# Performance work log

Hardware: AMD Instinct MI355X
Metric: run time of the kernel (lower is better)

## Reference

```python
import jax, jax.numpy as jnp
import numpy as np

B, T, TREF, C, H = 2, 2048, 512, 768, 12
D = C // H


def setup_inputs() -> dict:
    key = jax.random.key(0)
    ks = jax.random.split(key, 20)
    s = 0.02  # init scale for weights
    inp = {
        "x": jax.random.normal(ks[0], (B, T, C), dtype=jnp.float32),
        "mask": jax.random.randint(ks[1], (B, 1, T, T), 0, 2, dtype=jnp.int32),
        "rel_pos": jax.random.normal(ks[2], (H, T, T), dtype=jnp.float32) * 0.1,
        "ref_feat": jax.random.normal(ks[3], (B, TREF, C), dtype=jnp.float32),
    }
    names = ["Wq", "Wk", "Wv", "Wrk", "Wrv", "Wo"]
    for i, n in enumerate(names):
        inp[n] = jax.random.normal(ks[4 + i], (C, C), dtype=jnp.float32) * s
        inp["b" + n[1:]] = jnp.zeros((C,), dtype=jnp.float32)
    return inp


def _heads(t, W, b):
    # nn.Linear: y = t @ W.T + b, then (B, L, H, D) -> (B, H, L, D)
    Bt, L, _ = t.shape
    return (t @ W.T + b).reshape(Bt, L, H, D).transpose(0, 2, 1, 3)


def reference(x, mask, rel_pos, ref_feat, Wq, bq, Wk, bk, Wv, bv,
              Wrk, brk, Wrv, brv, Wo, bo):
    Bx, Tx, Cx = x.shape
    Tref = ref_feat.shape[1]
    q = _heads(x, Wq, bq)                  # (B,H,T,D)
    k = _heads(x, Wk, bk)
    v = _heads(x, Wv, bv)
    rk = _heads(ref_feat, Wrk, brk)        # (B,H,Tref,D)
    rv = _heads(ref_feat, Wrv, brv)
    k = jnp.concatenate([k, rk], axis=2)   # (B,H,T+Tref,D)
    v = jnp.concatenate([v, rv], axis=2)
    # additive bias: -inf where mask==1 (self keys), rel_pos on self keys,
    # ref keys get 0 bias (mask padded with 0)
    bias_self = jnp.where(mask == 1, -jnp.inf, 0.0).astype(x.dtype) + rel_pos[None]  # (B,H,T,T)
    bias = jnp.pad(bias_self, ((0, 0), (0, 0), (0, 0), (0, Tref)))  # (B,H,T,T+Tref)
    scale = 1.0 / jnp.sqrt(jnp.asarray(D, dtype=x.dtype))
    scores = jnp.einsum('bhqd,bhkd->bhqk', q, k) * scale + bias
    attn = jax.nn.softmax(scores, axis=-1)
    y = jnp.einsum('bhqk,bhkd->bhqd', attn, v)
    y = y.transpose(0, 2, 1, 3).reshape(Bx, Tx, Cx)
    return y @ Wo.T + bo
```

## Files before the change

kernel.cpp:

```cpp
#include <hip/hip_runtime.h>


typedef __bf16 bf16x8 __attribute__((ext_vector_type(8)));
typedef float floatx4 __attribute__((ext_vector_type(4)));

__device__ __forceinline__ ushort f2bf(float f) {
  uint u = __builtin_bit_cast(uint, f);
  return (ushort)((u + 0x7FFFu + ((u >> 16) & 1u)) >> 16);
}
__device__ __forceinline__ float bf2f(ushort u) {
  return __builtin_bit_cast(float, (uint)u << 16);
}

__device__ __forceinline__ void gld16(ushort* lds, const ushort* g) {
  __builtin_amdgcn_global_load_lds(
      (const __attribute__((address_space(1))) unsigned int*)g,
      (__attribute__((address_space(3))) unsigned int*)lds, 16, 0, 0);
}

__global__ __launch_bounds__(256) void cast_all(
    const float* __restrict__ x, const float* __restrict__ rf,
    const float* __restrict__ w0, const float* __restrict__ w1,
    const float* __restrict__ w2, const float* __restrict__ w3,
    const float* __restrict__ w4, const float* __restrict__ w5,
    ushort* __restrict__ dst) {
  size_t i4 = ((size_t)blockIdx.x * 256 + threadIdx.x) * 4;
  const float* src;
  size_t off;
  if (i4 < 3145728) { src = x; off = i4; }
  else if (i4 < 3932160) { src = rf; off = i4 - 3145728; }
  else {
    size_t r = i4 - 3932160;
    if (r < 589824) { src = w0; off = r; }
    else if (r < 2 * 589824) { src = w1; off = r - 589824; }
    else if (r < 3 * 589824) { src = w2; off = r - 2 * 589824; }
    else if (r < 4 * 589824) { src = w3; off = r - 3 * 589824; }
    else if (r < 5 * 589824) { src = w4; off = r - 4 * 589824; }
    else { src = w5; off = r - 5 * 589824; }
  }
  float4 v = *(const float4*)(src + off);
  ushort4 o;
  o.x = f2bf(v.x); o.y = f2bf(v.y); o.z = f2bf(v.z); o.w = f2bf(v.w);
  *(ushort4*)(dst + i4) = o;
}

__global__ __launch_bounds__(256) void pack_mask(
    const int* __restrict__ mask, unsigned long long* __restrict__ bits) {
  const int gid = blockIdx.x * 256 + threadIdx.x;
  const int4* src = (const int4*)(mask + (size_t)gid * 64);
  unsigned long long v = 0;
#pragma unroll
  for (int j = 0; j < 16; ++j) {
    int4 m = src[j];
    unsigned long long nib = (m.x ? 1ull : 0ull) | (m.y ? 2ull : 0ull) |
                             (m.z ? 4ull : 0ull) | (m.w ? 8ull : 0ull);
    v |= nib << (j * 4);
  }
  bits[gid] = v;
}

__device__ __forceinline__ void gemm_core(
    const ushort* __restrict__ Ab, const ushort* __restrict__ Bb,
    ushort* As, ushort* Bs, int tid, int quad, int l16, int mw, int nw,
    floatx4 acc[4][4]) {
  const int w = tid >> 6;
  const int r0 = tid >> 2, kp = (tid & 3) * 8;
  const size_t ga0 = (size_t)r0 * 768 + kp;
  const size_t ga1 = ga0 + (size_t)64 * 768;
#define GEMM_ISSUE(kb, p)                                   \
  do {                                                      \
    const int k0_ = (kb) * 32;                              \
    gld16(&As[(p) * 4096 + w * 512], Ab + ga0 + k0_);       \
    gld16(&As[(p) * 4096 + w * 512 + 2048], Ab + ga1 + k0_);\
    gld16(&Bs[(p) * 4096 + w * 512], Bb + ga0 + k0_);       \
    gld16(&Bs[(p) * 4096 + w * 512 + 2048], Bb + ga1 + k0_);\
  } while (0)
  GEMM_ISSUE(0, 0);
#pragma unroll 1
  for (int kb = 0; kb < 24; ++kb) {
    __syncthreads();
    if (kb < 23) GEMM_ISSUE(kb + 1, (kb + 1) & 1);
    const int p = kb & 1;
    bf16x8 af[4], bfr[4];
#pragma unroll
    for (int mt = 0; mt < 4; ++mt)
      af[mt] = *(const bf16x8*)&As[p * 4096 + (mw + mt * 16 + l16) * 32 + quad * 8];
#pragma unroll
    for (int nt = 0; nt < 4; ++nt)
      bfr[nt] = *(const bf16x8*)&Bs[p * 4096 + (nw + nt * 16 + l16) * 32 + quad * 8];
#pragma unroll
    for (int mt = 0; mt < 4; ++mt)
#pragma unroll
      for (int nt = 0; nt < 4; ++nt)
        acc[mt][nt] = __builtin_amdgcn_mfma_f32_16x16x32_bf16(af[mt], bfr[nt], acc[mt][nt], 0, 0, 0);
  }
#undef GEMM_ISSUE
}

template <int REF>
__global__ __launch_bounds__(256) void gemm_fused(
    const ushort* __restrict__ A, const ushort* __restrict__ W,
    const float* __restrict__ bA, const float* __restrict__ bB,
    const float* __restrict__ bC,
    ushort* __restrict__ oA, ushort* __restrict__ oB, ushort* __restrict__ oC) {
  const int bm = blockIdx.x, bn = blockIdx.y;
  const int tid = threadIdx.x;
  const int w = tid >> 6, lane = tid & 63, quad = lane >> 4, l16 = lane & 15;
  const int mw = (w >> 1) * 64, nw = (w & 1) * 64;

  __shared__ __align__(16) ushort As[2 * 4096];
  __shared__ __align__(16) ushort Bs[2 * 4096];

  floatx4 acc[4][4];
#pragma unroll
  for (int mt = 0; mt < 4; ++mt)
#pragma unroll
    for (int nt = 0; nt < 4; ++nt) acc[mt][nt] = (floatx4){0.f, 0.f, 0.f, 0.f};

  gemm_core(A + (size_t)bm * 128 * 768, W + (size_t)bn * 128 * 768,
            As, Bs, tid, quad, l16, mw, nw, acc);

  const int sec = bn / 6;
  const float* bp = sec == 0 ? bA : sec == 1 ? bB : bC;
  ushort* op = sec == 0 ? oA : sec == 1 ? oB : oC;
  const bool qlay = (REF == 0 && sec == 0);
#pragma unroll
  for (int nt = 0; nt < 4; ++nt) {
    const int nloc = (bn - sec * 6) * 128 + nw + nt * 16 + l16;
    const float bv = bp[nloc];
    const int hh = nloc >> 6, dd = nloc & 63;
#pragma unroll
    for (int mt = 0; mt < 4; ++mt)
#pragma unroll
      for (int i = 0; i < 4; ++i) {
        const int m = bm * 128 + mw + mt * 16 + quad * 4 + i;
        int bb, tt;
        if (REF == 0) { bb = m >> 11; tt = m & 2047; }
        else { bb = m >> 9; tt = (m & 511) + 2048; }
        const size_t idx = qlay ? (((size_t)(bb * 12 + hh) * 2048 + tt) * 64 + dd)
                                : (((size_t)(bb * 12 + hh) * 2560 + tt) * 64 + dd);
        op[idx] = f2bf(acc[mt][nt][i] + bv);
      }
  }
}

__global__ __launch_bounds__(256) void gemm_out(
    const ushort* __restrict__ A, const ushort* __restrict__ W,
    const float* __restrict__ bias, float* __restrict__ out) {
  const int bm = blockIdx.x, bn = blockIdx.y;
  const int tid = threadIdx.x;
  const int w = tid >> 6, lane = tid & 63, quad = lane >> 4, l16 = lane & 15;
  const int mw = (w >> 1) * 64, nw = (w & 1) * 64;

  __shared__ __align__(16) ushort As[2 * 4096];
  __shared__ __align__(16) ushort Bs[2 * 4096];

  floatx4 acc[4][4];
#pragma unroll
  for (int mt = 0; mt < 4; ++mt)
#pragma unroll
    for (int nt = 0; nt < 4; ++nt) acc[mt][nt] = (floatx4){0.f, 0.f, 0.f, 0.f};

  gemm_core(A + (size_t)bm * 128 * 768, W + (size_t)bn * 128 * 768,
            As, Bs, tid, quad, l16, mw, nw, acc);

#pragma unroll
  for (int nt = 0; nt < 4; ++nt) {
    const int n = bn * 128 + nw + nt * 16 + l16;
    const float bv = bias[n];
#pragma unroll
    for (int mt = 0; mt < 4; ++mt)
#pragma unroll
      for (int i = 0; i < 4; ++i) {
        const int m = bm * 128 + mw + mt * 16 + quad * 4 + i;
        out[(size_t)m * 768 + n] = acc[mt][nt][i] + bv;
      }
  }
}

__global__ __launch_bounds__(256, 3) void attn(
    const ushort* __restrict__ qb, const ushort* __restrict__ kb,
    const ushort* __restrict__ vb, const unsigned long long* __restrict__ bits,
    const float* __restrict__ relp, ushort* __restrict__ yb) {
  const int b = blockIdx.x, qt = blockIdx.y, h = blockIdx.z;
  const int tid = threadIdx.x;
  const int w = tid >> 6, lane = tid & 63, quad = lane >> 4, l16 = lane & 15;

  __shared__ __align__(16) ushort Kl[2][64 * 64];
  __shared__ __align__(16) ushort Vl[2][64 * 64];
  __shared__ __align__(16) ushort Rel[64 * 72];
  __shared__ __align__(16) ushort Ps[4][16 * 72];

  const ushort* qsrc = qb + ((size_t)(b * 12 + h) * 2048 + qt * 64) * 64;
  const ushort* ksrc = kb + (size_t)(b * 12 + h) * 2560 * 64;
  const ushort* vsrc = vb + (size_t)(b * 12 + h) * 2560 * 64;
  const int qrow = qt * 64 + w * 16 + l16;
  const unsigned long long* brow = bits + ((size_t)b * 2048 + qrow) * 32;
  const float* rbase = relp + ((size_t)h * 2048 + qt * 64) * 2048;

  const int krow = lane >> 3;
  const int kchunk = (lane & 7) ^ krow;

#pragma unroll
  for (int c = 0; c < 2; ++c) {
    const int f = tid + c * 256;
    *(uint4*)&Vl[1][(f >> 3) * 64 + (f & 7) * 8] = *(const uint4*)(qsrc + f * 8);
  }
#pragma unroll
  for (int c = 0; c < 2; ++c) {
    const int rb = w * 16 + c * 8;
    gld16(&Kl[0][rb * 64], ksrc + (rb + krow) * 64 + kchunk * 8);
  }
  uint4 vd[2];
  float4 rd[4];
  unsigned long long bnext;
  vd[0] = *(const uint4*)(vsrc + tid * 8);
  vd[1] = *(const uint4*)(vsrc + (tid + 256) * 8);
#pragma unroll
  for (int p = 0; p < 4; ++p) {
    const int idx = lane + p * 64, rr = idx >> 4, c4 = idx & 15;
    rd[p] = *(const float4*)(rbase + (size_t)(w * 16 + rr) * 2048 + c4 * 4);
  }
  bnext = brow[0];

  __syncthreads();
  bf16x8 bQ[2];
  bQ[0] = *(const bf16x8*)&Vl[1][(w * 16 + l16) * 64 + quad * 8];
  bQ[1] = *(const bf16x8*)&Vl[1][(w * 16 + l16) * 64 + 32 + quad * 8];

  floatx4 acc[4];
#pragma unroll
  for (int mt = 0; mt < 4; ++mt) acc[mt] = (floatx4){0.f, 0.f, 0.f, 0.f};
  float m_run = -__builtin_inff(), l_run = 0.f;

#pragma unroll 1
  for (int it = 0; it < 40; ++it) {
    const int p = it & 1;
    const bool self = it < 32;
#pragma unroll
    for (int c = 0; c < 2; ++c) {
      const int f = tid + c * 256;
      const int key = f >> 3, d0 = (f & 7) * 8;
      const int cb = (((key >> 3) ^ (f & 7)) & 7) * 8 + (key & 7);
      uint vv[4] = {vd[c].x, vd[c].y, vd[c].z, vd[c].w};
#pragma unroll
      for (int u = 0; u < 4; ++u) {
        Vl[p][(d0 + 2 * u) * 64 + cb] = (ushort)(vv[u] & 0xffffu);
        Vl[p][(d0 + 2 * u + 1) * 64 + cb] = (ushort)(vv[u] >> 16);
      }
    }
    if (self) {
#pragma unroll
      for (int pp = 0; pp < 4; ++pp) {
        const int idx = lane + pp * 64, rr = idx >> 4, c4 = idx & 15;
        ushort4 o;
        o.x = f2bf(rd[pp].x); o.y = f2bf(rd[pp].y);
        o.z = f2bf(rd[pp].z); o.w = f2bf(rd[pp].w);
        *(ushort4*)&Rel[(w * 16 + rr) * 72 + c4 * 4] = o;
      }
    }
    const unsigned long long bcur = bnext;
    __syncthreads();

    const int itn = it + 1;
    if (itn < 40) {
#pragma unroll
      for (int c = 0; c < 2; ++c) {
        const int rb = w * 16 + c * 8;
        gld16(&Kl[itn & 1][rb * 64], ksrc + (size_t)itn * 4096 + (rb + krow) * 64 + kchunk * 8);
      }
      const ushort* vt0 = vsrc + (size_t)itn * 4096;
      vd[0] = *(const uint4*)(vt0 + tid * 8);
      vd[1] = *(const uint4*)(vt0 + (tid + 256) * 8);
      if (itn < 32) {
#pragma unroll
        for (int pp = 0; pp < 4; ++pp) {
          const int idx = lane + pp * 64, rr = idx >> 4, c4 = idx & 15;
          rd[pp] = *(const float4*)(rbase + (size_t)(w * 16 + rr) * 2048 + itn * 64 + c4 * 4);
        }
        bnext = brow[itn];
      }
    }

    floatx4 st[4];
#pragma unroll
    for (int mt = 0; mt < 4; ++mt) st[mt] = (floatx4){0.f, 0.f, 0.f, 0.f};
#pragma unroll
    for (int kk = 0; kk < 2; ++kk)
#pragma unroll
      for (int mt = 0; mt < 4; ++mt) {
        const bf16x8 aK = *(const bf16x8*)
            &Kl[p][(mt * 16 + l16) * 64 + (((kk * 4 + quad) ^ (l16 & 7)) * 8)];
        st[mt] = __builtin_amdgcn_mfma_f32_16x16x32_bf16(aK, bQ[kk], st[mt], 0, 0, 0);
      }
#pragma unroll
    for (int mt = 0; mt < 4; ++mt) {
      if (self) {
        const ushort4 rv4 = *(const ushort4*)&Rel[(w * 16 + l16) * 72 + mt * 16 + quad * 4];
        const ushort rv[4] = {rv4.x, rv4.y, rv4.z, rv4.w};
#pragma unroll
        for (int i = 0; i < 4; ++i) {
          const float sv = st[mt][i] * 0.125f + bf2f(rv[i]);
          const int bit = mt * 16 + quad * 4 + i;
          st[mt][i] = ((bcur >> bit) & 1ull) ? -__builtin_inff() : sv;
        }
      } else {
#pragma unroll
        for (int i = 0; i < 4; ++i) st[mt][i] *= 0.125f;
      }
    }
    float tm = st[0][0];
#pragma unroll
    for (int mt = 0; mt < 4; ++mt)
#pragma unroll
      for (int i = 0; i < 4; ++i) tm = fmaxf(tm, st[mt][i]);
    tm = fmaxf(tm, __shfl_xor(tm, 16));
    tm = fmaxf(tm, __shfl_xor(tm, 32));
    const float mnew = fmaxf(m_run, tm);
    const float mref = (mnew == -__builtin_inff()) ? 0.f : mnew;
    const float alpha = (m_run == -__builtin_inff()) ? 0.f : __expf(m_run - mnew);
    float rs = 0.f;
#pragma unroll
    for (int mt = 0; mt < 4; ++mt)
#pragma unroll
      for (int i = 0; i < 4; ++i) {
        const float pv = __expf(st[mt][i] - mref);
        st[mt][i] = pv;
        rs += pv;
      }
    rs += __shfl_xor(rs, 16);
    rs += __shfl_xor(rs, 32);
    l_run = l_run * alpha + rs;
    m_run = mnew;
#pragma unroll
    for (int mt = 0; mt < 4; ++mt)
#pragma unroll
      for (int i = 0; i < 4; ++i) acc[mt][i] *= alpha;

    {
      ushort* pw = &Ps[w][l16 * 72 + quad * 4];
#pragma unroll
      for (int mt = 0; mt < 4; ++mt) {
        const uint pk0 = (uint)f2bf(st[mt][0]) | ((uint)f2bf(st[mt][1]) << 16);
        const uint pk1 = (uint)f2bf(st[mt][2]) | ((uint)f2bf(st[mt][3]) << 16);
        *(uint*)&pw[mt * 16] = pk0;
        *(uint*)&pw[mt * 16 + 2] = pk1;
      }
    }
#pragma unroll
    for (int kk = 0; kk < 2; ++kk) {
      const bf16x8 bP = *(const bf16x8*)&Ps[w][l16 * 72 + kk * 32 + quad * 8];
#pragma unroll
      for (int mt = 0; mt < 4; ++mt) {
        const int dd = mt * 16 + l16;
        const int cs = (((kk * 4 + quad) ^ (dd >> 3)) & 7) * 8;
        const bf16x8 aV = *(const bf16x8*)&Vl[p][dd * 64 + cs];
        acc[mt] = __builtin_amdgcn_mfma_f32_16x16x32_bf16(aV, bP, acc[mt], 0, 0, 0);
      }
    }
  }

  const float inv = 1.f / l_run;
  ushort* yrow = yb + ((size_t)b * 2048 + qt * 64 + w * 16 + l16) * 768 + h * 64;
#pragma unroll
  for (int mt = 0; mt < 4; ++mt)
#pragma unroll
    for (int i = 0; i < 4; ++i)
      yrow[mt * 16 + quad * 4 + i] = f2bf(acc[mt][i] * inv);
}

extern "C" void kernel_launch(void* const* d_in, const int* in_sizes, int n_in,
                              void* d_out, int out_size, void* d_ws, size_t ws_size,
                              hipStream_t stream) {
  const float* x = (const float*)d_in[0];
  const int* mask = (const int*)d_in[1];
  const float* relp = (const float*)d_in[2];
  const float* ref = (const float*)d_in[3];
  const float* Wq = (const float*)d_in[4];
  const float* bq = (const float*)d_in[5];
  const float* Wk = (const float*)d_in[6];
  const float* bk = (const float*)d_in[7];
  const float* Wv = (const float*)d_in[8];
  const float* bv = (const float*)d_in[9];
  const float* Wrk = (const float*)d_in[10];
  const float* brk = (const float*)d_in[11];
  const float* Wrv = (const float*)d_in[12];
  const float* brv = (const float*)d_in[13];
  const float* Wo = (const float*)d_in[14];
  const float* bo = (const float*)d_in[15];

  ushort* xb = (ushort*)d_ws;
  ushort* refb = xb + 3145728;
  ushort* wb = refb + 786432;
  ushort* qbuf = wb + 6 * 589824;
  ushort* kbuf = qbuf + 3145728;
  ushort* vbuf = kbuf + 3932160;
  ushort* ybuf = vbuf + 3932160;
  unsigned long long* bitsbuf = (unsigned long long*)(ybuf + 3145728);

  cast_all<<<7296, 256, 0, stream>>>(x, ref, Wq, Wk, Wv, Wrk, Wrv, Wo, xb);
  pack_mask<<<512, 256, 0, stream>>>(mask, bitsbuf);

  gemm_fused<0><<<dim3(32, 18), 256, 0, stream>>>(
      xb, wb, bq, bk, bv, qbuf, kbuf, vbuf);
  gemm_fused<1><<<dim3(8, 12), 256, 0, stream>>>(
      refb, wb + (size_t)3 * 589824, brk, brv, nullptr, kbuf, vbuf, nullptr);

  attn<<<dim3(2, 32, 12), 256, 0, stream>>>(qbuf, kbuf, vbuf, bitsbuf, relp, ybuf);

  gemm_out<<<dim3(32, 6), 256, 0, stream>>>(
      ybuf, wb + (size_t)5 * 589824, bo, (float*)d_out);
}
```

Before: 474.2 us.

## Store V transposed in projection, fold softmax scale into Q, use exp2 with lazy rescale

The QKV projection epilogue now writes V in a transposed (head, d, token) layout, so the attention kernel can load V tiles straight into LDS with async global_load_lds instead of scattering them through registers. Q is pre-multiplied by scale*log2(e), so the scores go directly to exp2, and rel_pos is read per lane from global memory instead of being staged as bf16 in LDS. Online-softmax rescaling is skipped when the running max grows by at most 8, which saves the exp and the accumulator multiplies but lets unnormalized values grow larger in float. The P tile layout in LDS is also reorganized, and the Q tile is loaded directly from global memory.

Measured after the change: 488.6 us. 3.0% more time.

```diff
diff --git a/kernel.cpp b/kernel.cpp
--- a/kernel.cpp
+++ b/kernel.cpp
@@ -3,13 +3,25 @@
 
 typedef __bf16 bf16x8 __attribute__((ext_vector_type(8)));
 typedef float floatx4 __attribute__((ext_vector_type(4)));
+typedef uint uintx2 __attribute__((ext_vector_type(2)));
 
 __device__ __forceinline__ ushort f2bf(float f) {
   uint u = __builtin_bit_cast(uint, f);
   return (ushort)((u + 0x7FFFu + ((u >> 16) & 1u)) >> 16);
 }
-__device__ __forceinline__ float bf2f(ushort u) {
-  return __builtin_bit_cast(float, (uint)u << 16);
+
+__device__ __forceinline__ uint pack2bf(float lo, float hi) {
+  ushort a = __builtin_bit_cast(ushort, (__bf16)lo);
+  ushort b = __builtin_bit_cast(ushort, (__bf16)hi);
+  return (uint)a | ((uint)b << 16);
+}
+
+__device__ __forceinline__ float fexp2(float x) {
+#if __has_builtin(__builtin_amdgcn_exp2f)
+  return __builtin_amdgcn_exp2f(x);
+#else
+  return exp2f(x);
+#endif
 }
 
 __device__ __forceinline__ void gld16(ushort* lds, const ushort* g) {
@@ -124,23 +136,41 @@
   const float* bp = sec == 0 ? bA : sec == 1 ? bB : bC;
   ushort* op = sec == 0 ? oA : sec == 1 ? oB : oC;
   const bool qlay = (REF == 0 && sec == 0);
+  const bool vlay = (REF == 0) ? (sec == 2) : (sec == 1);
+  const float scl = qlay ? 0.18033688011112042f : 1.0f;
 #pragma unroll
   for (int nt = 0; nt < 4; ++nt) {
     const int nloc = (bn - sec * 6) * 128 + nw + nt * 16 + l16;
     const float bv = bp[nloc];
     const int hh = nloc >> 6, dd = nloc & 63;
-#pragma unroll
-    for (int mt = 0; mt < 4; ++mt)
-#pragma unroll
-      for (int i = 0; i < 4; ++i) {
-        const int m = bm * 128 + mw + mt * 16 + quad * 4 + i;
-        int bb, tt;
-        if (REF == 0) { bb = m >> 11; tt = m & 2047; }
-        else { bb = m >> 9; tt = (m & 511) + 2048; }
-        const size_t idx = qlay ? (((size_t)(bb * 12 + hh) * 2048 + tt) * 64 + dd)
-                                : (((size_t)(bb * 12 + hh) * 2560 + tt) * 64 + dd);
-        op[idx] = f2bf(acc[mt][nt][i] + bv);
-      }
+    if (vlay) {
+#pragma unroll
+      for (int mt = 0; mt < 4; ++mt) {
+        const int m0 = bm * 128 + mw + mt * 16 + quad * 4;
+        int bb, t0;
+        if (REF == 0) { bb = m0 >> 11; t0 = m0 & 2047; }
+        else { bb = m0 >> 9; t0 = (m0 & 511) + 2048; }
+        ushort4 o;
+        o.x = f2bf(acc[mt][nt][0] + bv);
+        o.y = f2bf(acc[mt][nt][1] + bv);
+        o.z = f2bf(acc[mt][nt][2] + bv);
+        o.w = f2bf(acc[mt][nt][3] + bv);
+        *(ushort4*)&op[((size_t)(bb * 12 + hh) * 64 + dd) * 2560 + t0] = o;
+      }
+    } else {
+#pragma unroll
+      for (int mt = 0; mt < 4; ++mt)
+#pragma unroll
+        for (int i = 0; i < 4; ++i) {
+          const int m = bm * 128 + mw + mt * 16 + quad * 4 + i;
+          int bb, tt;
+          if (REF == 0) { bb = m >> 11; tt = m & 2047; }
+          else { bb = m >> 9; tt = (m & 511) + 2048; }
+          const size_t idx = qlay ? (((size_t)(bb * 12 + hh) * 2048 + tt) * 64 + dd)
+                                  : (((size_t)(bb * 12 + hh) * 2560 + tt) * 64 + dd);
+          op[idx] = f2bf((acc[mt][nt][i] + bv) * scl);
+        }
+    }
   }
 }
 
@@ -186,47 +216,36 @@
   const int tid = threadIdx.x;
   const int w = tid >> 6, lane = tid & 63, quad = lane >> 4, l16 = lane & 15;
 
-  __shared__ __align__(16) ushort Kl[2][64 * 64];
-  __shared__ __align__(16) ushort Vl[2][64 * 64];
-  __shared__ __align__(16) ushort Rel[64 * 72];
-  __shared__ __align__(16) ushort Ps[4][16 * 72];
+  __shared__ __align__(16) ushort Kl[2][4096];
+  __shared__ __align__(16) ushort Vtl[2][4096];
+  __shared__ __align__(16) ushort Ps[4][8][16][8];
 
   const ushort* qsrc = qb + ((size_t)(b * 12 + h) * 2048 + qt * 64) * 64;
   const ushort* ksrc = kb + (size_t)(b * 12 + h) * 2560 * 64;
-  const ushort* vsrc = vb + (size_t)(b * 12 + h) * 2560 * 64;
+  const ushort* vtsrc = vb + (size_t)(b * 12 + h) * 64 * 2560;
   const int qrow = qt * 64 + w * 16 + l16;
   const unsigned long long* brow = bits + ((size_t)b * 2048 + qrow) * 32;
-  const float* rbase = relp + ((size_t)h * 2048 + qt * 64) * 2048;
+  const float* rrow = relp + ((size_t)h * 2048 + qrow) * 2048;
 
   const int krow = lane >> 3;
   const int kchunk = (lane & 7) ^ krow;
 
-#pragma unroll
-  for (int c = 0; c < 2; ++c) {
-    const int f = tid + c * 256;
-    *(uint4*)&Vl[1][(f >> 3) * 64 + (f & 7) * 8] = *(const uint4*)(qsrc + f * 8);
-  }
 #pragma unroll
   for (int c = 0; c < 2; ++c) {
     const int rb = w * 16 + c * 8;
     gld16(&Kl[0][rb * 64], ksrc + (rb + krow) * 64 + kchunk * 8);
-  }
-  uint4 vd[2];
+    gld16(&Vtl[0][rb * 64], vtsrc + (size_t)(rb + krow) * 2560 + kchunk * 8);
+  }
+
+  bf16x8 bQ[2];
+  bQ[0] = *(const bf16x8*)(qsrc + (w * 16 + l16) * 64 + quad * 8);
+  bQ[1] = *(const bf16x8*)(qsrc + (w * 16 + l16) * 64 + 32 + quad * 8);
+
   float4 rd[4];
-  unsigned long long bnext;
-  vd[0] = *(const uint4*)(vsrc + tid * 8);
-  vd[1] = *(const uint4*)(vsrc + (tid + 256) * 8);
-#pragma unroll
-  for (int p = 0; p < 4; ++p) {
-    const int idx = lane + p * 64, rr = idx >> 4, c4 = idx & 15;
-    rd[p] = *(const float4*)(rbase + (size_t)(w * 16 + rr) * 2048 + c4 * 4);
-  }
-  bnext = brow[0];
-
-  __syncthreads();
-  bf16x8 bQ[2];
-  bQ[0] = *(const bf16x8*)&Vl[1][(w * 16 + l16) * 64 + quad * 8];
-  bQ[1] = *(const bf16x8*)&Vl[1][(w * 16 + l16) * 64 + 32 + quad * 8];
+#pragma unroll
+  for (int mt = 0; mt < 4; ++mt)
+    rd[mt] = *(const float4*)(rrow + mt * 16 + quad * 4);
+  unsigned long long bnext = brow[0];
 
   floatx4 acc[4];
 #pragma unroll
@@ -237,48 +256,19 @@
   for (int it = 0; it < 40; ++it) {
     const int p = it & 1;
     const bool self = it < 32;
-#pragma unroll
-    for (int c = 0; c < 2; ++c) {
-      const int f = tid + c * 256;
-      const int key = f >> 3, d0 = (f & 7) * 8;
-      const int cb = (((key >> 3) ^ (f & 7)) & 7) * 8 + (key & 7);
-      uint vv[4] = {vd[c].x, vd[c].y, vd[c].z, vd[c].w};
-#pragma unroll
-      for (int u = 0; u < 4; ++u) {
-        Vl[p][(d0 + 2 * u) * 64 + cb] = (ushort)(vv[u] & 0xffffu);
-        Vl[p][(d0 + 2 * u + 1) * 64 + cb] = (ushort)(vv[u] >> 16);
-      }
-    }
-    if (self) {
-#pragma unroll
-      for (int pp = 0; pp < 4; ++pp) {
-        const int idx = lane + pp * 64, rr = idx >> 4, c4 = idx & 15;
-        ushort4 o;
-        o.x = f2bf(rd[pp].x); o.y = f2bf(rd[pp].y);
-        o.z = f2bf(rd[pp].z); o.w = f2bf(rd[pp].w);
-        *(ushort4*)&Rel[(w * 16 + rr) * 72 + c4 * 4] = o;
-      }
-    }
     const unsigned long long bcur = bnext;
     __syncthreads();
 
     const int itn = it + 1;
     if (itn < 40) {
+      const int pn = itn & 1;
 #pragma unroll
       for (int c = 0; c < 2; ++c) {
         const int rb = w * 16 + c * 8;
-        gld16(&Kl[itn & 1][rb * 64], ksrc + (size_t)itn * 4096 + (rb + krow) * 64 + kchunk * 8);
-      }
-      const ushort* vt0 = vsrc + (size_t)itn * 4096;
-      vd[0] = *(const uint4*)(vt0 + tid * 8);
-      vd[1] = *(const uint4*)(vt0 + (tid + 256) * 8);
-      if (itn < 32) {
-#pragma unroll
-        for (int pp = 0; pp < 4; ++pp) {
-          const int idx = lane + pp * 64, rr = idx >> 4, c4 = idx & 15;
-          rd[pp] = *(const float4*)(rbase + (size_t)(w * 16 + rr) * 2048 + itn * 64 + c4 * 4);
-        }
-        bnext = brow[itn];
+        gld16(&Kl[pn][rb * 64],
+              ksrc + (size_t)itn * 4096 + (rb + krow) * 64 + kchunk * 8);
+        gld16(&Vtl[pn][rb * 64],
+              vtsrc + (size_t)(rb + krow) * 2560 + itn * 64 + kchunk * 8);
       }
     }
 
@@ -293,69 +283,79 @@
             &Kl[p][(mt * 16 + l16) * 64 + (((kk * 4 + quad) ^ (l16 & 7)) * 8)];
         st[mt] = __builtin_amdgcn_mfma_f32_16x16x32_bf16(aK, bQ[kk], st[mt], 0, 0, 0);
       }
-#pragma unroll
-    for (int mt = 0; mt < 4; ++mt) {
-      if (self) {
-        const ushort4 rv4 = *(const ushort4*)&Rel[(w * 16 + l16) * 72 + mt * 16 + quad * 4];
-        const ushort rv[4] = {rv4.x, rv4.y, rv4.z, rv4.w};
+
+    if (self) {
+#pragma unroll
+      for (int mt = 0; mt < 4; ++mt) {
+        const float rr[4] = {rd[mt].x, rd[mt].y, rd[mt].z, rd[mt].w};
+        const uint ni = (uint)(bcur >> (mt * 16 + quad * 4)) & 0xFu;
 #pragma unroll
         for (int i = 0; i < 4; ++i) {
-          const float sv = st[mt][i] * 0.125f + bf2f(rv[i]);
-          const int bit = mt * 16 + quad * 4 + i;
-          st[mt][i] = ((bcur >> bit) & 1ull) ? -__builtin_inff() : sv;
+          const float sv = fmaf(rr[i], 1.4426950408889634f, st[mt][i]);
+          st[mt][i] = (ni & (1u << i)) ? -__builtin_inff() : sv;
         }
-      } else {
-#pragma unroll
-        for (int i = 0; i < 4; ++i) st[mt][i] *= 0.125f;
-      }
-    }
-    float tm = st[0][0];
-#pragma unroll
-    for (int mt = 0; mt < 4; ++mt)
-#pragma unroll
-      for (int i = 0; i < 4; ++i) tm = fmaxf(tm, st[mt][i]);
+      }
+    }
+    if (itn < 32) {
+#pragma unroll
+      for (int mt = 0; mt < 4; ++mt)
+        rd[mt] = *(const float4*)(rrow + itn * 64 + mt * 16 + quad * 4);
+      bnext = brow[itn];
+    }
+
+    float tm = fmaxf(fmaxf(st[0][0], st[0][1]), fmaxf(st[0][2], st[0][3]));
+#pragma unroll
+    for (int mt = 1; mt < 4; ++mt)
+      tm = fmaxf(tm, fmaxf(fmaxf(st[mt][0], st[mt][1]), fmaxf(st[mt][2], st[mt][3])));
     tm = fmaxf(tm, __shfl_xor(tm, 16));
     tm = fmaxf(tm, __shfl_xor(tm, 32));
-    const float mnew = fmaxf(m_run, tm);
-    const float mref = (mnew == -__builtin_inff()) ? 0.f : mnew;
-    const float alpha = (m_run == -__builtin_inff()) ? 0.f : __expf(m_run - mnew);
+    float mref;
+    if (__all(tm - m_run <= 8.f)) {
+      mref = m_run;
+    } else {
+      const float mnew = fmaxf(m_run, tm);
+      mref = (mnew == -__builtin_inff()) ? 0.f : mnew;
+      const float alpha =
+          (m_run == -__builtin_inff()) ? 0.f : fexp2(m_run - mnew);
+      m_run = mnew;
+      l_run *= alpha;
+#pragma unroll
+      for (int mt = 0; mt < 4; ++mt) acc[mt] *= alpha;
+    }
     float rs = 0.f;
 #pragma unroll
     for (int mt = 0; mt < 4; ++mt)
 #pragma unroll
       for (int i = 0; i < 4; ++i) {
-        const float pv = __expf(st[mt][i] - mref);
+        const float pv = fexp2(st[mt][i] - mref);
         st[mt][i] = pv;
         rs += pv;
       }
     rs += __shfl_xor(rs, 16);
     rs += __shfl_xor(rs, 32);
-    l_run = l_run * alpha + rs;
-    m_run = mnew;
-#pragma unroll
-    for (int mt = 0; mt < 4; ++mt)
-#pragma unroll
-      for (int i = 0; i < 4; ++i) acc[mt][i] *= alpha;
+    l_run += rs;
 
     {
-      ushort* pw = &Ps[w][l16 * 72 + quad * 4];
+      ushort* pwb = &Ps[w][quad >> 1][l16][(quad & 1) * 4];
 #pragma unroll
       for (int mt = 0; mt < 4; ++mt) {
-        const uint pk0 = (uint)f2bf(st[mt][0]) | ((uint)f2bf(st[mt][1]) << 16);
-        const uint pk1 = (uint)f2bf(st[mt][2]) | ((uint)f2bf(st[mt][3]) << 16);
-        *(uint*)&pw[mt * 16] = pk0;
-        *(uint*)&pw[mt * 16 + 2] = pk1;
-      }
-    }
+        uintx2 pkv;
+        pkv.x = pack2bf(st[mt][0], st[mt][1]);
+        pkv.y = pack2bf(st[mt][2], st[mt][3]);
+        *(uintx2*)(pwb + mt * 256) = pkv;
+      }
+    }
+
+    const bf16x8 bP0 = *(const bf16x8*)&Ps[w][quad][l16][0];
+    const bf16x8 bP1 = *(const bf16x8*)&Ps[w][4 + quad][l16][0];
 #pragma unroll
     for (int kk = 0; kk < 2; ++kk) {
-      const bf16x8 bP = *(const bf16x8*)&Ps[w][l16 * 72 + kk * 32 + quad * 8];
+      const bf16x8 bPk = kk ? bP1 : bP0;
 #pragma unroll
       for (int mt = 0; mt < 4; ++mt) {
-        const int dd = mt * 16 + l16;
-        const int cs = (((kk * 4 + quad) ^ (dd >> 3)) & 7) * 8;
-        const bf16x8 aV = *(const bf16x8*)&Vl[p][dd * 64 + cs];
-        acc[mt] = __builtin_amdgcn_mfma_f32_16x16x32_bf16(aV, bP, acc[mt], 0, 0, 0);
+        const bf16x8 aV = *(const bf16x8*)
+            &Vtl[p][(mt * 16 + l16) * 64 + (((kk * 4 + quad) ^ (l16 & 7)) * 8)];
+        acc[mt] = __builtin_amdgcn_mfma_f32_16x16x32_bf16(aV, bPk, acc[mt], 0, 0, 0);
       }
     }
   }
```
